# Optimization experiments

Hardware: AMD Instinct MI355X
Metric: run time of the kernel (lower is better)

## Reference

```python
import jax, jax.numpy as jnp
import numpy as np

B, N, O, H, A = 4096, 8, 64, 64, 16  # batch, agents, obs_dim, hx_size, actions
GH = 2 * H  # GRU input/hidden size = 128


def setup_inputs() -> dict:
    key = jax.random.key(0)
    ks = jax.random.split(key, 14)
    s = lambda *sh: 1.0 / np.sqrt(sh[-1])
    obs = jax.random.normal(ks[0], (B, N, O), dtype=jnp.float32)
    u = jax.random.uniform(ks[1], (B, N, N, 2), minval=1e-6, maxval=1.0 - 1e-6)
    gumbel = -jnp.log(-jnp.log(u))  # standard Gumbel noise, precomputed for determinism
    W1 = jax.random.normal(ks[2], (N, O, 128)) * s(O)
    b1 = jnp.zeros((N, 128), jnp.float32)
    W2 = jax.random.normal(ks[3], (N, 128, H)) * s(128)
    b2 = jnp.zeros((N, H), jnp.float32)
    # per ordered pair (i,j): single-step GRU cell, input GH, hidden GH
    Wi = jax.random.normal(ks[4], (N, N, 3 * GH, GH)) * s(GH)
    bi = jax.random.normal(ks[5], (N, N, 3 * GH)) * 0.01
    bh = jax.random.normal(ks[6], (N, N, 3 * GH)) * 0.01
    # gate head: GH -> 2 logits (G2ANet hard attention)
    Wg = jax.random.normal(ks[7], (N, N, 2, GH)) * s(GH)
    bg = jnp.zeros((N, N, 2), jnp.float32)
    # decode: concat(h_i, other_i) (2H) -> actions
    Wd = jax.random.normal(ks[8], (N, A, 2 * H)) * s(2 * H)
    bd = jnp.zeros((N, A), jnp.float32)
    return {"obs": obs, "gumbel": gumbel, "W1": W1, "b1": b1, "W2": W2, "b2": b2,
            "Wi": Wi, "bi": bi, "bh": bh, "Wg": Wg, "bg": bg, "Wd": Wd, "bd": bd}


def _forward(obs, gumbel, W1, b1, W2, b2, Wi, bi, bh, Wg, bg, Wd, bd):
    n = obs.shape[1]
    # per-agent encode MLP: [B,N,O] -> [B,N,H]
    h = jax.nn.relu(jnp.einsum('bno,noh->bnh', obs, W1) + b1)
    h = jax.nn.relu(jnp.einsum('bnh,nhk->bnk', h, W2) + b2)
    # pairwise input u[b,i,j] = concat(h_i, h_j)  -> [B,N,N,2H]
    bsz = h.shape[0]
    hi = jnp.broadcast_to(h[:, :, None, :], (bsz, n, n, H))
    hj = jnp.broadcast_to(h[:, None, :, :], (bsz, n, n, H))
    u = jnp.concatenate([hi, hj], axis=-1)
    # single-step GRU cell with zero initial hidden (Wh @ h0 == 0)
    gates = jnp.einsum('bijc,ijgc->bijg', u, Wi) + bi  # [B,N,N,3*GH]
    gr, gz, gn = jnp.split(gates, 3, axis=-1)
    br, bz, bn = jnp.split(bh, 3, axis=-1)
    r = jax.nn.sigmoid(gr + br)
    z = jax.nn.sigmoid(gz + bz)
    nn_ = jnp.tanh(gn + r * bn)
    g = (1.0 - z) * nn_  # GRU output, [B,N,N,GH]
    # 2-way gumbel-softmax, hard (straight-through)
    logits = jnp.einsum('bijc,ijoc->bijo', g, Wg) + bg  # [B,N,N,2]
    y_soft = jax.nn.softmax(logits + gumbel, axis=-1)  # tau = 1
    y_hard = jax.nn.one_hot(jnp.argmax(y_soft, axis=-1), 2, dtype=y_soft.dtype)
    y = jax.lax.stop_gradient(y_hard - y_soft) + y_soft
    w = y[..., 1] * (1.0 - jnp.eye(n, dtype=y.dtype))  # exclude self, [B,N,N]
    # gated aggregation of other agents' hiddens
    other = jnp.einsum('bij,bjh->bih', w, h)  # [B,N,H]
    comm = jnp.concatenate([h, other], axis=-1)  # [B,N,2H]
    q = jnp.einsum('bnc,nac->bna', comm, Wd) + bd  # [B,N,A]
    return q


def reference(obs, gumbel, W1, b1, W2, b2, Wi, bi, bh, Wg, bg, Wd, bd):
    return _forward(obs, gumbel, W1, b1, W2, b2, Wi, bi, bh, Wg, bg, Wd, bd)
```

## Files before the change

### kernel.cpp

```cpp
#include <hip/hip_runtime.h>

#define BATCH 4096
#define NAG   8
#define OBS   64
#define HD    64
#define GH    128
#define NACT  16
#define TAU   0.025f
#define CAP   16384

typedef short  bf16x8 __attribute__((ext_vector_type(8)));
typedef unsigned short u16x8 __attribute__((ext_vector_type(8)));
typedef float  f32x4  __attribute__((ext_vector_type(4)));

__device__ __forceinline__ float fast_sigmoid(float x) {
    return 1.f / (1.f + __expf(-x));
}
__device__ __forceinline__ float sigmoid_negarg(float x) {
    return 1.f / (1.f + __expf(x));
}
__device__ __forceinline__ float fast_tanh(float x) {
    x = fminf(fmaxf(x, -15.f), 15.f);
    const float e = __expf(2.f * x);
    return (e - 1.f) / (e + 1.f);
}
__device__ __forceinline__ unsigned short f2bf(float f) {
    unsigned int u = __builtin_bit_cast(unsigned int, f);
    u = (u + 0x7FFFu + ((u >> 16) & 1u)) >> 16;
    return (unsigned short)u;
}

__global__ void zero_counter(int* c) { if (threadIdx.x == 0) c[0] = 0; }

__global__ __launch_bounds__(128) void bprep_kernel(
    const float* __restrict__ bi, const float* __restrict__ bh,
    const float* __restrict__ Wg, float* __restrict__ econst)
{
    const int pp = blockIdx.x;
    const int pi = pp / 7;
    int pj = pp % 7; pj += (pj >= pi);
    const int pb = pi * NAG + pj;
    const int c  = threadIdx.x;
    econst[0*8192 + pb*128 + c] = bi[pb*384 + c]       + bh[pb*384 + c];
    econst[1*8192 + pb*128 + c] = bi[pb*384 + 128 + c] + bh[pb*384 + 128 + c];
    econst[2*8192 + pb*128 + c] = bi[pb*384 + 256 + c];
    econst[3*8192 + pb*128 + c] = bh[pb*384 + 256 + c];
    econst[4*8192 + pb*128 + c] = Wg[pb*256 + 128 + c] - Wg[pb*256 + c];
}

__global__ __launch_bounds__(256) void wiconv_kernel(
    const float* __restrict__ Wi, unsigned short* __restrict__ wib)
{
    const int t   = blockIdx.x * 256 + threadIdx.x;
    const int pp  = t / 6144;
    const int rem = t - pp * 6144;
    const int gp  = rem >> 4;
    const int k8  = rem & 15;
    const int pi  = pp / 7;
    int pj = pp % 7; pj += (pj >= pi);
    const int pb  = pi * NAG + pj;
    const int cg  = gp / 48;
    const int r2  = gp - cg * 48;
    const int s   = r2 >> 4, cl = r2 & 15;
    const int g   = s * GH + cg * 16 + cl;
    const float* src = Wi + ((size_t)pb * 384 + g) * GH + k8 * 8;
    u16x8 o;
#pragma unroll
    for (int e = 0; e < 8; ++e) o[e] = f2bf(src[e]);
    *reinterpret_cast<u16x8*>(wib + ((size_t)pb * 384 + gp) * GH + k8 * 8) = o;
}

__global__ __launch_bounds__(256, 2) void encode_kernel(
    const float* __restrict__ obs, const float* __restrict__ W1,
    const float* __restrict__ b1, const float* __restrict__ W2,
    const float* __restrict__ b2, float* __restrict__ h,
    unsigned short* __restrict__ hb)
{
    const int n    = blockIdx.x >> 6;
    const int tile = blockIdx.x & 63;
    const int b0   = tile * 64;
    const int tid  = threadIdx.x;

    __shared__ float u1[OBS * 68];
    __shared__ float h1t[GH * 68];
    __shared__ float wl[16 * GH];

    const float* __restrict__ W1n = W1 + n * (OBS * GH);
    const float* __restrict__ W2n = W2 + n * (GH * HD);
    const float* __restrict__ b1n = b1 + n * GH;
    const float* __restrict__ b2n = b2 + n * HD;

    {
        const int c  = tid & 63;
        const int r0 = tid >> 6;
        for (int rr = 0; rr < 16; ++rr) {
            const int bb = r0 * 16 + rr;
            u1[c * 68 + bb] = obs[((size_t)(b0 + bb) * NAG + n) * OBS + c];
        }
    }

    const int bq = tid & 15;
    const int cg = tid >> 4;

    float acc1[8][4];
#pragma unroll
    for (int cc = 0; cc < 8; ++cc)
#pragma unroll
        for (int bb = 0; bb < 4; ++bb) acc1[cc][bb] = 0.f;

    for (int kc = 0; kc < 4; ++kc) {
        __syncthreads();
#pragma unroll
        for (int p = 0; p < 2; ++p) {
            const int f = tid + p * 256;
            const int k = f >> 5, c4 = f & 31;
            *reinterpret_cast<float4*>(&wl[k * GH + c4 * 4]) =
                *reinterpret_cast<const float4*>(&W1n[(kc * 16 + k) * GH + c4 * 4]);
        }
        __syncthreads();
#pragma unroll 2
        for (int k = 0; k < 16; ++k) {
            const float4 uu = *reinterpret_cast<const float4*>(
                &u1[(kc * 16 + k) * 68 + bq * 4]);
            const float ub[4] = {uu.x, uu.y, uu.z, uu.w};
            const float4 wa = *reinterpret_cast<const float4*>(&wl[k * GH + cg * 8]);
            const float4 wb = *reinterpret_cast<const float4*>(&wl[k * GH + cg * 8 + 4]);
            const float wv[8] = {wa.x, wa.y, wa.z, wa.w, wb.x, wb.y, wb.z, wb.w};
#pragma unroll
            for (int cc = 0; cc < 8; ++cc)
#pragma unroll
                for (int bb = 0; bb < 4; ++bb)
                    acc1[cc][bb] += wv[cc] * ub[bb];
        }
    }

    {
        const float4 ba  = *reinterpret_cast<const float4*>(&b1n[cg * 8]);
        const float4 bb4 = *reinterpret_cast<const float4*>(&b1n[cg * 8 + 4]);
        const float bv[8] = {ba.x, ba.y, ba.z, ba.w, bb4.x, bb4.y, bb4.z, bb4.w};
#pragma unroll
        for (int cc = 0; cc < 8; ++cc)
#pragma unroll
            for (int bb = 0; bb < 4; ++bb)
                h1t[(cg * 8 + cc) * 68 + bq * 4 + bb] =
                    fmaxf(acc1[cc][bb] + bv[cc], 0.f);
    }

    const int og = tid >> 4;
    float acc2[4][4];
#pragma unroll
    for (int oc = 0; oc < 4; ++oc)
#pragma unroll
        for (int bb = 0; bb < 4; ++bb) acc2[oc][bb] = 0.f;

    for (int kc = 0; kc < 8; ++kc) {
        __syncthreads();
        {
            const int k = tid >> 4, o4 = tid & 15;
            *reinterpret_cast<float4*>(&wl[k * HD + o4 * 4]) =
                *reinterpret_cast<const float4*>(&W2n[(kc * 16 + k) * HD + o4 * 4]);
        }
        __syncthreads();
#pragma unroll 2
        for (int k = 0; k < 16; ++k) {
            const float4 uu = *reinterpret_cast<const float4*>(
                &h1t[(kc * 16 + k) * 68 + bq * 4]);
            const float ub[4] = {uu.x, uu.y, uu.z, uu.w};
            const float4 wa = *reinterpret_cast<const float4*>(&wl[k * HD + og * 4]);
            const float wv[4] = {wa.x, wa.y, wa.z, wa.w};
#pragma unroll
            for (int oc = 0; oc < 4; ++oc)
#pragma unroll
                for (int bb = 0; bb < 4; ++bb)
                    acc2[oc][bb] += wv[oc] * ub[bb];
        }
    }

    {
        const float4 b2v = *reinterpret_cast<const float4*>(&b2n[og * 4]);
#pragma unroll
        for (int bb = 0; bb < 4; ++bb) {
            float4 o;
            o.x = fmaxf(acc2[0][bb] + b2v.x, 0.f);
            o.y = fmaxf(acc2[1][bb] + b2v.y, 0.f);
            o.z = fmaxf(acc2[2][bb] + b2v.z, 0.f);
            o.w = fmaxf(acc2[3][bb] + b2v.w, 0.f);
            const size_t row = (size_t)(b0 + bq * 4 + bb) * NAG + n;
            *reinterpret_cast<float4*>(&h[row * HD + og * 4]) = o;
            ushort4 hv;
            hv.x = f2bf(o.x); hv.y = f2bf(o.y); hv.z = f2bf(o.z); hv.w = f2bf(o.w);
            *reinterpret_cast<ushort4*>(&hb[row * HD + og * 4]) = hv;
        }
    }
}

__global__ __launch_bounds__(512, 3) void pair_mfma_kernel(
    const unsigned short* __restrict__ hb, const unsigned short* __restrict__ wib,
    const float* __restrict__ econst, const float* __restrict__ bg,
    const float* __restrict__ gum, float* __restrict__ wout,
    int* __restrict__ list, int* __restrict__ counter)
{
    const int pairp = blockIdx.x >> 6;
    const int tile  = blockIdx.x & 63;
    const int pi = pairp / 7;
    int pj = pairp % 7; pj += (pj >= pi);
    const int pb = pi * NAG + pj;
    const int b0 = tile * 64;

    const int tid = threadIdx.x;
    const int wv  = tid >> 6;
    const int g   = wv & 3;
    const int hh  = wv >> 2;
    const int l   = tid & 63;
    const int cl  = l & 15;
    const int rg  = l >> 4;

    f32x4 acc[2][6];
#pragma unroll
    for (int bb = 0; bb < 2; ++bb)
#pragma unroll
        for (int t = 0; t < 6; ++t) acc[bb][t] = (f32x4){0.f, 0.f, 0.f, 0.f};

    const size_t wbase = ((size_t)pb * 384 + g * 96 + cl) * GH + rg * 8;

#define LOADA(dst, kb_) { \
    const int ag = ((kb_) < 2) ? pi : pj; \
    const int ch = ((kb_) & 1) * 32 + rg * 8; \
    _Pragma("unroll") \
    for (int bb = 0; bb < 2; ++bb) { \
        const int b = b0 + (2 * hh + bb) * 16 + cl; \
        dst[bb] = *reinterpret_cast<const bf16x8*>( \
            &hb[((size_t)b * NAG + ag) * HD + ch]); } }

#define LOADB(dst, kb_) { \
    _Pragma("unroll") \
    for (int t = 0; t < 6; ++t) \
        dst[t] = *reinterpret_cast<const bf16x8*>( \
            &wib[wbase + (size_t)(kb_) * 32 + (size_t)t * 16 * GH]); }

#define MFMA6(a_, b_) { \
    _Pragma("unroll") \
    for (int t = 0; t < 6; ++t) \
    _Pragma("unroll") \
    for (int bb = 0; bb < 2; ++bb) \
        acc[bb][t] = __builtin_amdgcn_mfma_f32_16x16x32_bf16( \
            a_[bb], b_[t], acc[bb][t], 0, 0, 0); }

    bf16x8 av0[2], av1[2], bv0[6], bv1[6];
    LOADA(av0, 0); LOADB(bv0, 0);
    LOADA(av1, 1); LOADB(bv1, 1);
    MFMA6(av0, bv0);
    LOADA(av0, 2); LOADB(bv0, 2);
    MFMA6(av1, bv1);
    LOADA(av1, 3); LOADB(bv1, 3);
    MFMA6(av0, bv0);
    MFMA6(av1, bv1);
#undef LOADA
#undef LOADB
#undef MFMA6

    __shared__ float part[64][69];
    __shared__ float part2[64][9];
    float pl[2][4];
#pragma unroll
    for (int bb = 0; bb < 2; ++bb)
#pragma unroll
        for (int r = 0; r < 4; ++r) pl[bb][r] = 0.f;

#pragma unroll
    for (int cgl = 0; cgl < 2; ++cgl) {
        const int c  = (2 * g + cgl) * 16 + cl;
        const float br  = econst[0 * 8192 + pb * 128 + c];
        const float bz  = econst[1 * 8192 + pb * 128 + c];
        const float bn  = econst[2 * 8192 + pb * 128 + c];
        const float bhn = econst[3 * 8192 + pb * 128 + c];
        const float dw  = econst[4 * 8192 + pb * 128 + c];
#pragma unroll
        for (int bb = 0; bb < 2; ++bb)
#pragma unroll
            for (int r = 0; r < 4; ++r) {
                const float rr  = fast_sigmoid(acc[bb][cgl * 3 + 0][r] + br);
                const float omz = sigmoid_negarg(acc[bb][cgl * 3 + 1][r] + bz);
                const float nn  = fast_tanh(acc[bb][cgl * 3 + 2][r] + bn + rr * bhn);
                pl[bb][r] += omz * nn * dw;
            }
    }
#pragma unroll
    for (int bb = 0; bb < 2; ++bb)
#pragma unroll
        for (int r = 0; r < 4; ++r)
            part[g * 16 + cl][(2 * hh + bb) * 16 + rg * 4 + r] = pl[bb][r];
    __syncthreads();

    {
        const int row = tid & 63, seg = tid >> 6;
        float s = 0.f;
#pragma unroll
        for (int t = 0; t < 8; ++t) s += part[seg * 8 + t][row];
        part2[row][seg] = s;
    }
    __syncthreads();

    if (tid < 64) {
        float s = 0.f;
#pragma unroll
        for (int t = 0; t < 8; ++t) s += part2[tid][t];
        const int b = b0 + tid;
        const float dbg = bg[pb * 2 + 1] - bg[pb * 2 + 0];
        const float* gp2 = gum + ((size_t)(b * NAG + pi) * NAG + pj) * 2;
        const float margin = s + dbg + (gp2[1] - gp2[0]);
        wout[(b * NAG + pi) * NAG + pj] = (margin > 0.f) ? 1.f : 0.f;
        if (fabsf(margin) < TAU) {
            const int idx = atomicAdd(counter, 1);
            if (idx < CAP) list[idx] = (b << 6) | (pi << 3) | pj;
        }
    }
}

__global__ __launch_bounds__(256) void refine_kernel(
    const float* __restrict__ h, const float* __restrict__ Wi,
    const float* __restrict__ bi, const float* __restrict__ bh,
    const float* __restrict__ Wg, const float* __restrict__ bg,
    const float* __restrict__ gum, const int* __restrict__ list,
    const int* __restrict__ counter, float* __restrict__ wout)
{
    __shared__ float u_sh[128];
    __shared__ float part[384 * 9];
    __shared__ float pl_sh[128];

    const int tid = threadIdx.x;
    const int rs  = tid >> 3;
    const int fs  = tid & 7;
    int count = counter[0]; if (count > CAP) count = CAP;

    for (int e = blockIdx.x; e < count; e += gridDim.x) {
        const int code = list[e];
        const int b = code >> 6, pi2 = (code >> 3) & 7, pj2 = code & 7;
        const int pb = pi2 * NAG + pj2;
        const float* __restrict__ Wr = Wi + (size_t)pb * 384 * GH;

        if (tid < 32) {
            const float* src = (tid < 16)
                ? h + ((size_t)b * NAG + pi2) * HD + tid * 4
                : h + ((size_t)b * NAG + pj2) * HD + (tid - 16) * 4;
            *reinterpret_cast<float4*>(&u_sh[tid * 4]) =
                *reinterpret_cast<const float4*>(src);
        }
        __syncthreads();

        float4 uv[4];
#pragma unroll
        for (int s = 0; s < 4; ++s)
            uv[s] = *reinterpret_cast<const float4*>(&u_sh[(fs + 8 * s) * 4]);

#pragma unroll 2
        for (int si = 0; si < 12; ++si) {
            const int r = si * 32 + rs;
            const float* row = Wr + (size_t)r * GH;
            float p = 0.f;
#pragma unroll
            for (int s = 0; s < 4; ++s) {
                const float4 wv = *reinterpret_cast<const float4*>(
                    row + (fs + 8 * s) * 4);
                p += wv.x * uv[s].x + wv.y * uv[s].y
                   + wv.z * uv[s].z + wv.w * uv[s].w;
            }
            part[r * 9 + fs] = p;
        }
        __syncthreads();

        if (tid < 128) {
            const int c = tid;
            float gr = 0.f, gz = 0.f, gn = 0.f;
#pragma unroll
            for (int k = 0; k < 8; ++k) {
                gr += part[c * 9 + k];
                gz += part[(128 + c) * 9 + k];
                gn += part[(256 + c) * 9 + k];
            }
            const float r = fast_sigmoid(gr + bi[pb*384 + c] + bh[pb*384 + c]);
            const float z = fast_sigmoid(gz + bi[pb*384 + 128 + c] + bh[pb*384 + 128 + c]);
            const float n = fast_tanh(gn + bi[pb*384 + 256 + c]
                                      + r * bh[pb*384 + 256 + c]);
            pl_sh[c] = (1.f - z) * n * (Wg[pb*256 + 128 + c] - Wg[pb*256 + c]);
        }
        __syncthreads();

        if (tid < 64) {
            float p = pl_sh[tid] + pl_sh[tid + 64];
#pragma unroll
            for (int m = 1; m < 64; m <<= 1) p += __shfl_xor(p, m, 64);
            if (tid == 0) {
                const float dbg = bg[pb * 2 + 1] - bg[pb * 2 + 0];
                const float* gp2 = gum + ((size_t)(b * NAG + pi2) * NAG + pj2) * 2;
                const float margin = p + dbg + (gp2[1] - gp2[0]);
                wout[(b * NAG + pi2) * NAG + pj2] = (margin > 0.f) ? 1.f : 0.f;
            }
        }
        __syncthreads();
    }
}

__global__ __launch_bounds__(256, 2) void agg_kernel(
    const float* __restrict__ h, const float* __restrict__ w,
    const float* __restrict__ Wd, const float* __restrict__ bd,
    float* __restrict__ q)
{
    const int b0 = blockIdx.x * 8;
    __shared__ float hl[8 * 520];
    const int tid = threadIdx.x;
#pragma unroll
    for (int p = 0; p < 4; ++p) {
        const int f = tid + p * 256;
        const int r = f >> 7, cc = (f & 127) * 4;
        *reinterpret_cast<float4*>(&hl[r * 520 + cc]) =
            *reinterpret_cast<const float4*>(&h[(size_t)b0 * 512 + f * 4]);
    }
    __syncthreads();

    const int aq = tid & 3;
    const int i  = (tid >> 2) & 7;
    const int bb = tid >> 5;
    const int b  = b0 + bb;

    float other[HD];
#pragma unroll
    for (int c = 0; c < HD; ++c) other[c] = 0.f;
    const float* wrow = w + ((size_t)b * NAG + i) * NAG;
    for (int j = 0; j < NAG; ++j) {
        if (j == i) continue;
        const float wv = wrow[j];
        const float* hr = &hl[bb * 520 + j * 64];
#pragma unroll
        for (int c4 = 0; c4 < HD / 4; ++c4) {
            const float4 v = *reinterpret_cast<const float4*>(hr + c4 * 4);
            other[c4*4+0] += wv * v.x; other[c4*4+1] += wv * v.y;
            other[c4*4+2] += wv * v.z; other[c4*4+3] += wv * v.w;
        }
    }
    const float* hi = &hl[bb * 520 + i * 64];
    const float* __restrict__ Wdp = Wd + (i * NACT) * (2 * HD);
    float qo[4];
#pragma unroll
    for (int t = 0; t < 4; ++t) {
        const int a = aq * 4 + t;
        float acc0 = bd[i * NACT + a];
        const float* wr = Wdp + a * 2 * HD;
#pragma unroll
        for (int c4 = 0; c4 < HD / 4; ++c4) {
            const float4 w1 = *reinterpret_cast<const float4*>(wr + c4 * 4);
            const float4 w2 = *reinterpret_cast<const float4*>(wr + 64 + c4 * 4);
            acc0 += hi[c4*4+0] * w1.x + hi[c4*4+1] * w1.y
                  + hi[c4*4+2] * w1.z + hi[c4*4+3] * w1.w
                  + other[c4*4+0] * w2.x + other[c4*4+1] * w2.y
                  + other[c4*4+2] * w2.z + other[c4*4+3] * w2.w;
        }
        qo[t] = acc0;
    }
    float4 qv = {qo[0], qo[1], qo[2], qo[3]};
    *reinterpret_cast<float4*>(&q[((size_t)b * NAG + i) * NACT + aq * 4]) = qv;
}

extern "C" void kernel_launch(void* const* d_in, const int* in_sizes, int n_in,
                              void* d_out, int out_size, void* d_ws, size_t ws_size,
                              hipStream_t stream) {
    const float* obs = (const float*)d_in[0];
    const float* gum = (const float*)d_in[1];
    const float* W1  = (const float*)d_in[2];
    const float* b1  = (const float*)d_in[3];
    const float* W2  = (const float*)d_in[4];
    const float* b2  = (const float*)d_in[5];
    const float* Wi  = (const float*)d_in[6];
    const float* bi  = (const float*)d_in[7];
    const float* bh  = (const float*)d_in[8];
    const float* Wg  = (const float*)d_in[9];
    const float* bg  = (const float*)d_in[10];
    const float* Wd  = (const float*)d_in[11];
    const float* bd  = (const float*)d_in[12];
    float* q = (float*)d_out;

    float*          ws     = (float*)d_ws;
    float*          h      = ws;
    float*          w      = ws + 2097152;
    unsigned short* hb     = (unsigned short*)(ws + 2359296);
    unsigned short* wib    = (unsigned short*)(ws + 3407872);
    int*            list   = (int*)(ws + 4980736);
    int*            cnt    = (int*)(ws + 4997120);
    float*          econst = ws + 4997184;

    hipLaunchKernelGGL(zero_counter, dim3(1), dim3(64), 0, stream, cnt);
    hipLaunchKernelGGL(bprep_kernel, dim3(56), dim3(128), 0, stream,
                       bi, bh, Wg, econst);
    hipLaunchKernelGGL(wiconv_kernel, dim3(1344), dim3(256), 0, stream, Wi, wib);
    hipLaunchKernelGGL(encode_kernel, dim3(NAG * (BATCH / 64)), dim3(256), 0, stream,
                       obs, W1, b1, W2, b2, h, hb);
    hipLaunchKernelGGL(pair_mfma_kernel, dim3(56 * 64), dim3(512), 0, stream,
                       hb, wib, econst, bg, gum, w, list, cnt);
    hipLaunchKernelGGL(refine_kernel, dim3(2048), dim3(256), 0, stream,
                       h, Wi, bi, bh, Wg, bg, gum, list, cnt, w);
    hipLaunchKernelGGL(agg_kernel, dim3(BATCH / 8), dim3(256), 0, stream,
                       h, w, Wd, bd, q);
}
```

Measured before the change: 293.7 us.

## Re-tile pair GRU MFMA per wave to 16 channels by 64 rows, faster activations

Each wave now owns one 16-channel group (all three gates) across all 64 batch rows, instead of a 2-channel-group by 32-row split. Each wave loads 3 B fragments and 4 A fragments per k-step rather than 6 and 2. The shared-memory partial buffer grows to 128 channels, each element is written directly, and the reduction now sums 16 rows per segment. Sigmoid and tanh use the hardware reciprocal intrinsic and a single-exp tanh without clamping, and the occupancy hint drops from 3 to 2 blocks per SM. The trade-off is a larger LDS footprint and slightly lower precision.

```diff
diff --git a/kernel.cpp b/kernel.cpp
--- a/kernel.cpp
+++ b/kernel.cpp
@@ -16,13 +16,19 @@
 __device__ __forceinline__ float fast_sigmoid(float x) {
     return 1.f / (1.f + __expf(-x));
 }
-__device__ __forceinline__ float sigmoid_negarg(float x) {
-    return 1.f / (1.f + __expf(x));
-}
 __device__ __forceinline__ float fast_tanh(float x) {
     x = fminf(fmaxf(x, -15.f), 15.f);
     const float e = __expf(2.f * x);
     return (e - 1.f) / (e + 1.f);
+}
+__device__ __forceinline__ float fsig(float x) {
+    return __builtin_amdgcn_rcpf(1.f + __expf(-x));
+}
+__device__ __forceinline__ float fsig_neg(float x) {
+    return __builtin_amdgcn_rcpf(1.f + __expf(x));
+}
+__device__ __forceinline__ float ftanh(float x) {
+    return 1.f - 2.f * __builtin_amdgcn_rcpf(1.f + __expf(2.f * x));
 }
 __device__ __forceinline__ unsigned short f2bf(float f) {
     unsigned int u = __builtin_bit_cast(unsigned int, f);
@@ -194,7 +200,7 @@
     }
 }
 
-__global__ __launch_bounds__(512, 3) void pair_mfma_kernel(
+__global__ __launch_bounds__(512, 2) void pair_mfma_kernel(
     const unsigned short* __restrict__ hb, const unsigned short* __restrict__ wib,
     const float* __restrict__ econst, const float* __restrict__ bg,
     const float* __restrict__ gum, float* __restrict__ wout,
@@ -209,102 +215,88 @@
 
     const int tid = threadIdx.x;
     const int wv  = tid >> 6;
-    const int g   = wv & 3;
-    const int hh  = wv >> 2;
     const int l   = tid & 63;
     const int cl  = l & 15;
     const int rg  = l >> 4;
 
-    f32x4 acc[2][6];
-#pragma unroll
-    for (int bb = 0; bb < 2; ++bb)
-#pragma unroll
-        for (int t = 0; t < 6; ++t) acc[bb][t] = (f32x4){0.f, 0.f, 0.f, 0.f};
-
-    const size_t wbase = ((size_t)pb * 384 + g * 96 + cl) * GH + rg * 8;
+    f32x4 acc[4][3];
+#pragma unroll
+    for (int bt = 0; bt < 4; ++bt)
+#pragma unroll
+        for (int t = 0; t < 3; ++t) acc[bt][t] = (f32x4){0.f, 0.f, 0.f, 0.f};
+
+    const size_t wbase = ((size_t)pb * 384 + wv * 48 + cl) * GH + rg * 8;
 
 #define LOADA(dst, kb_) { \
     const int ag = ((kb_) < 2) ? pi : pj; \
     const int ch = ((kb_) & 1) * 32 + rg * 8; \
     _Pragma("unroll") \
-    for (int bb = 0; bb < 2; ++bb) { \
-        const int b = b0 + (2 * hh + bb) * 16 + cl; \
-        dst[bb] = *reinterpret_cast<const bf16x8*>( \
+    for (int bt = 0; bt < 4; ++bt) { \
+        const int b = b0 + bt * 16 + cl; \
+        dst[bt] = *reinterpret_cast<const bf16x8*>( \
             &hb[((size_t)b * NAG + ag) * HD + ch]); } }
 
 #define LOADB(dst, kb_) { \
     _Pragma("unroll") \
-    for (int t = 0; t < 6; ++t) \
+    for (int t = 0; t < 3; ++t) \
         dst[t] = *reinterpret_cast<const bf16x8*>( \
             &wib[wbase + (size_t)(kb_) * 32 + (size_t)t * 16 * GH]); }
 
-#define MFMA6(a_, b_) { \
+#define MFMA3(a_, b_) { \
     _Pragma("unroll") \
-    for (int t = 0; t < 6; ++t) \
+    for (int t = 0; t < 3; ++t) \
     _Pragma("unroll") \
-    for (int bb = 0; bb < 2; ++bb) \
-        acc[bb][t] = __builtin_amdgcn_mfma_f32_16x16x32_bf16( \
-            a_[bb], b_[t], acc[bb][t], 0, 0, 0); }
-
-    bf16x8 av0[2], av1[2], bv0[6], bv1[6];
+    for (int bt = 0; bt < 4; ++bt) \
+        acc[bt][t] = __builtin_amdgcn_mfma_f32_16x16x32_bf16( \
+            a_[bt], b_[t], acc[bt][t], 0, 0, 0); }
+
+    bf16x8 av0[4], av1[4], bv0[3], bv1[3];
     LOADA(av0, 0); LOADB(bv0, 0);
     LOADA(av1, 1); LOADB(bv1, 1);
-    MFMA6(av0, bv0);
+    MFMA3(av0, bv0);
     LOADA(av0, 2); LOADB(bv0, 2);
-    MFMA6(av1, bv1);
+    MFMA3(av1, bv1);
     LOADA(av1, 3); LOADB(bv1, 3);
-    MFMA6(av0, bv0);
-    MFMA6(av1, bv1);
+    MFMA3(av0, bv0);
+    MFMA3(av1, bv1);
 #undef LOADA
 #undef LOADB
-#undef MFMA6
-
-    __shared__ float part[64][69];
-    __shared__ float part2[64][9];
-    float pl[2][4];
-#pragma unroll
-    for (int bb = 0; bb < 2; ++bb)
-#pragma unroll
-        for (int r = 0; r < 4; ++r) pl[bb][r] = 0.f;
-
-#pragma unroll
-    for (int cgl = 0; cgl < 2; ++cgl) {
-        const int c  = (2 * g + cgl) * 16 + cl;
+#undef MFMA3
+
+    __shared__ float part[128 * 69];
+    __shared__ float part2[64 * 9];
+    {
+        const int c   = wv * 16 + cl;
         const float br  = econst[0 * 8192 + pb * 128 + c];
         const float bz  = econst[1 * 8192 + pb * 128 + c];
         const float bn  = econst[2 * 8192 + pb * 128 + c];
         const float bhn = econst[3 * 8192 + pb * 128 + c];
         const float dw  = econst[4 * 8192 + pb * 128 + c];
 #pragma unroll
-        for (int bb = 0; bb < 2; ++bb)
+        for (int bt = 0; bt < 4; ++bt)
 #pragma unroll
             for (int r = 0; r < 4; ++r) {
-                const float rr  = fast_sigmoid(acc[bb][cgl * 3 + 0][r] + br);
-                const float omz = sigmoid_negarg(acc[bb][cgl * 3 + 1][r] + bz);
-                const float nn  = fast_tanh(acc[bb][cgl * 3 + 2][r] + bn + rr * bhn);
-                pl[bb][r] += omz * nn * dw;
+                const float rr  = fsig(acc[bt][0][r] + br);
+                const float omz = fsig_neg(acc[bt][1][r] + bz);
+                const float nn  = ftanh(acc[bt][2][r] + bn + rr * bhn);
+                part[c * 69 + bt * 16 + rg * 4 + r] = omz * nn * dw;
             }
     }
-#pragma unroll
-    for (int bb = 0; bb < 2; ++bb)
-#pragma unroll
-        for (int r = 0; r < 4; ++r)
-            part[g * 16 + cl][(2 * hh + bb) * 16 + rg * 4 + r] = pl[bb][r];
     __syncthreads();
 
     {
         const int row = tid & 63, seg = tid >> 6;
         float s = 0.f;
 #pragma unroll
-        for (int t = 0; t < 8; ++t) s += part[seg * 8 + t][row];
-        part2[row][seg] = s;
+        for (int t = 0; t < 16; ++t) s += part[(seg * 16 + t) * 69 + row];
+        part2[row * 9 + seg] = s;
     }
     __syncthreads();
 
     if (tid < 64) {
         float s = 0.f;
 #pragma unroll
-        for (int t = 0; t < 8; ++t) s += part2[tid][t];
+        for (int t = 0; t < 8; ++t) s += part2[tid * 9 + t];
         const int b = b0 + tid;
         const float dbg = bg[pb * 2 + 1] - bg[pb * 2 + 0];
         const float* gp2 = gum + ((size_t)(b * NAG + pi) * NAG + pj) * 2;
```

Measured after the change: 268.5 us. 8.6% less time.
